# Performance work log

Hardware: AMD Instinct MI355X
Metric: run time of the kernel (lower is better)

The kernel has to match this reference:

```python
import jax, jax.numpy as jnp
import numpy as np

G = 8          # n_games
D_IN = 512     # per-game input dim (equal for all games)
H1 = 1024
H2 = 1024
A = 128        # max_actions
B = 8192       # batch rows


def setup_inputs() -> dict:
    key = jax.random.key(0)
    ks = jax.random.split(key, 9)
    state = jax.random.normal(ks[0], (B, D_IN), dtype=jnp.float32)
    idx = jax.random.randint(ks[1], (B,), 0, G, dtype=jnp.int32)
    # per-game input linears: uniform(-1/sqrt(fan_in), 1/sqrt(fan_in))
    lim1 = 1.0 / np.sqrt(D_IN)
    W1 = jax.random.uniform(ks[2], (G, D_IN, H1), minval=-lim1, maxval=lim1, dtype=jnp.float32)
    b1 = jax.random.uniform(ks[3], (G, H1), minval=-lim1, maxval=lim1, dtype=jnp.float32)
    # shared linear
    lim2 = 1.0 / np.sqrt(H1)
    W2 = jax.random.uniform(ks[4], (H1, H2), minval=-lim2, maxval=lim2, dtype=jnp.float32)
    b2 = jax.random.uniform(ks[5], (H2,), minval=-lim2, maxval=lim2, dtype=jnp.float32)
    # per-game output heads: uniform(-0.003, 0.003)
    W3 = jax.random.uniform(ks[6], (G, H2, A), minval=-0.003, maxval=0.003, dtype=jnp.float32)
    b3 = jax.random.uniform(ks[7], (G, A), minval=-0.003, maxval=0.003, dtype=jnp.float32)
    return {"state": state, "idx": idx, "W1": W1, "b1": b1, "W2": W2, "b2": b2, "W3": W3, "b3": b3}


def reference(state, idx, W1, b1, W2, b2, W3, b3):
    # Torch code concatenates per-game groups in sorted-unique-idx order,
    # i.e. a stable permutation of rows by idx; reproduce exactly.
    perm = jnp.argsort(idx, stable=True)          # [B]
    s = state[perm]                               # [B, D_IN]
    g = idx[perm]                                 # [B] game of each permuted row
    # routed first layer: compute all games then gather per-row game
    h1_all = jnp.einsum('bd,gdh->bgh', s, W1) + b1            # [B, G, H1]
    h1 = jax.nn.relu(jnp.take_along_axis(h1_all, g[:, None, None], axis=1)[:, 0, :])  # [B, H1]
    h_f = jax.nn.relu(h1 @ W2 + b2)                            # [B, H2]
    a = jnp.tanh(jnp.einsum('bh,gha->bga', h_f, W3) + b3)      # [B, G, A]
    # NOTE: original gathers heads with the ORIGINAL (unpermuted) idx,
    # even though rows of `a` are in permuted order. Reproduce faithfully.
    out = jnp.take_along_axis(a, idx[:, None, None], axis=1)[:, 0, :]  # [B, A]
    return out
```

## Files before the change

### kernel.cpp

```cpp
#include <hip/hip_runtime.h>
#include <math.h>

#define G_GAMES 8
#define D_IN 512
#define H1 1024
#define H2 1024
#define A_DIM 128
#define B_ROWS 8192

typedef short bf16x8 __attribute__((ext_vector_type(8)));
typedef float f32x4 __attribute__((ext_vector_type(4)));

#define WS_OFF   0u
#define WS_PERM  256u
#define WS_SPERM 33280u
#define WS_W1T   (WS_SPERM + B_ROWS*D_IN*2u)
#define WS_W2T   (WS_W1T + G_GAMES*D_IN*H1*2u)
#define WS_W3T   (WS_W2T + (unsigned)H1*H2*2u)
#define WS_H1    (WS_W3T + G_GAMES*H2*A_DIM*2u)
#define WS_HF    WS_SPERM

__device__ __forceinline__ unsigned short f2bf(float x) {
  union { float f; unsigned int u; } v; v.f = x;
  unsigned int r = v.u + 0x7fffu + ((v.u >> 16) & 1u);
  return (unsigned short)(r >> 16);
}

__device__ __forceinline__ void async_load16(const void* gptr, void* ldsptr) {
  __builtin_amdgcn_global_load_lds(
      (const __attribute__((address_space(1))) unsigned int*)gptr,
      (__attribute__((address_space(3))) unsigned int*)ldsptr,
      16, 0, 0);
}

__global__ __launch_bounds__(1024) void k_sort(const int* __restrict__ idx,
                                               int* __restrict__ perm,
                                               int* __restrict__ off) {
  __shared__ int wtot[16][9];
  __shared__ int wbase[16][9];
  __shared__ int offs[9];
  const int t = threadIdx.x;
  const int lane = t & 63, wave = t >> 6;
  int my[8];
  {
    const int4 a = *(const int4*)(idx + t * 8);
    const int4 b = *(const int4*)(idx + t * 8 + 4);
    my[0] = a.x; my[1] = a.y; my[2] = a.z; my[3] = a.w;
    my[4] = b.x; my[5] = b.y; my[6] = b.z; my[7] = b.w;
  }
  int local[8] = {0,0,0,0,0,0,0,0};
#pragma unroll
  for (int i = 0; i < 8; ++i) local[my[i]]++;
  int incl[8];
#pragma unroll
  for (int g = 0; g < 8; ++g) {
    int v = local[g];
#pragma unroll
    for (int d = 1; d < 64; d <<= 1) {
      const int n = __shfl_up(v, d);
      if (lane >= d) v += n;
    }
    incl[g] = v;
  }
  if (lane == 63) {
#pragma unroll
    for (int g = 0; g < 8; ++g) wtot[wave][g] = incl[g];
  }
  __syncthreads();
  if (t < 8) {
    int s = 0;
#pragma unroll
    for (int w = 0; w < 16; ++w) { wbase[w][t] = s; s += wtot[w][t]; }
    wtot[0][t] = s;
  }
  __syncthreads();
  if (t == 0) {
    int s = 0;
#pragma unroll
    for (int g = 0; g < 8; ++g) { offs[g] = s; off[g] = s; s += wtot[0][g]; }
    offs[8] = s; off[8] = s;
  }
  __syncthreads();
  int start[8];
#pragma unroll
  for (int g = 0; g < 8; ++g)
    start[g] = offs[g] + wbase[wave][g] + (incl[g] - local[g]);
#pragma unroll
  for (int i = 0; i < 8; ++i) {
    const int g = my[i];
    perm[start[g]++] = t * 8 + i;
  }
}

__device__ __forceinline__ void trans_tile(const float* __restrict__ in,
                                           unsigned short* __restrict__ out,
                                           int R, int C, int xt, int yt, int z) {
  in  += (size_t)z * R * C;
  out += (size_t)z * R * C;
  __shared__ float tile[64][65];
  const int c0 = xt * 64, r0 = yt * 64;
  const int tx = threadIdx.x & 63, ty = threadIdx.x >> 6;
#pragma unroll
  for (int rr = ty; rr < 64; rr += 4)
    tile[rr][tx] = in[(size_t)(r0 + rr) * C + c0 + tx];
  __syncthreads();
#pragma unroll
  for (int cc = ty; cc < 64; cc += 4)
    out[(size_t)(c0 + cc) * R + r0 + tx] = f2bf(tile[tx][cc]);
}

__global__ __launch_bounds__(256) void k_prep(const float* __restrict__ W1,
                                              const float* __restrict__ W2,
                                              const float* __restrict__ W3,
                                              const float* __restrict__ state,
                                              const int* __restrict__ perm,
                                              unsigned short* __restrict__ W1T,
                                              unsigned short* __restrict__ W2T,
                                              unsigned short* __restrict__ W3T,
                                              unsigned short* __restrict__ sPerm) {
  const int b = blockIdx.x;
  if (b < 1024) {
    const int z = b >> 7, r = b & 127;
    trans_tile(W1, W1T, D_IN, H1, r & 15, r >> 4, z);
  } else if (b < 1280) {
    const int r = b - 1024;
    trans_tile(W2, W2T, H1, H2, r & 15, r >> 4, 0);
  } else if (b < 1536) {
    const int r = (b - 1280) & 31, z = (b - 1280) >> 5;
    trans_tile(W3, W3T, H2, A_DIM, r & 1, r >> 1, z);
  } else {
    const int bb = b - 1536;
    const int p = bb * 2 + (threadIdx.x >> 7);
    const int c = (threadIdx.x & 127) << 2;
    const int src = perm[p];
    const float4 v = *(const float4*)(state + (size_t)src * D_IN + c);
    ushort4 o;
    o.x = f2bf(v.x); o.y = f2bf(v.y); o.z = f2bf(v.z); o.w = f2bf(v.w);
    *(ushort4*)(sPerm + (size_t)p * D_IN + c) = o;
  }
}

__device__ __forceinline__ void gemm_mfma_core(const unsigned short* const* aRow,
                                               const unsigned short* const* bRow,
                                               unsigned short* ldsA, unsigned short* ldsB,
                                               int KTOT, int tid, f32x4 acc[4][4]) {
  const int lane = tid & 63;
  const int wave = tid >> 6;
  const int wm = wave & 1, wn = wave >> 1;
  const int gcol = ((lane & 7) ^ (lane >> 3)) << 3;
  char* ldsAc = (char*)ldsA;
  char* ldsBc = (char*)ldsB;
  const int mA = wm * 64 + (lane & 15);
  const int nB = wn * 64 + (lane & 15);
  const int kq = (lane >> 4) & 3;
  const int swz = lane & 7;
  for (int k0 = 0; k0 < KTOT; k0 += 64) {
    __syncthreads();
#pragma unroll
    for (int c = 0; c < 4; ++c) {
      const int ldsRow = wave * 32 + c * 8;
      async_load16(aRow[c] + k0 + gcol, ldsAc + ldsRow * 128);
      async_load16(bRow[c] + k0 + gcol, ldsBc + ldsRow * 128);
    }
    __syncthreads();
#pragma unroll
    for (int ks = 0; ks < 2; ++ks) {
      bf16x8 aF[4], bF[4];
      const int u = ((((ks << 2) + kq) ^ swz) << 4);
#pragma unroll
      for (int i = 0; i < 4; ++i)
        aF[i] = *(const bf16x8*)(ldsAc + (mA + i * 16) * 128 + u);
#pragma unroll
      for (int j = 0; j < 4; ++j)
        bF[j] = *(const bf16x8*)(ldsBc + (nB + j * 16) * 128 + u);
#pragma unroll
      for (int i = 0; i < 4; ++i)
#pragma unroll
        for (int j = 0; j < 4; ++j)
          acc[i][j] = __builtin_amdgcn_mfma_f32_16x16x32_bf16(aF[i], bF[j], acc[i][j], 0, 0, 0);
    }
  }
}

__device__ __forceinline__ bool seg_map(const int* __restrict__ off, int T,
                                        int& g, int& seg1, int& row0) {
  int base = 0;
  for (int gg = 0; gg < 8; ++gg) {
    const int s = off[gg], e = off[gg + 1];
    const int nt = (e - s + 127) >> 7;
    if (T < base + nt) { g = gg; seg1 = e; row0 = s + (T - base) * 128; return true; }
    base += nt;
  }
  return false;
}

__device__ __forceinline__ bool seg_map32(const int* __restrict__ off, int T,
                                          int& g, int& seg1, int& row0) {
  int base = 0;
  for (int gg = 0; gg < 8; ++gg) {
    const int s = off[gg], e = off[gg + 1];
    const int nt = (e - s + 31) >> 5;
    if (T < base + nt) { g = gg; seg1 = e; row0 = s + (T - base) * 32; return true; }
    base += nt;
  }
  return false;
}

__global__ __launch_bounds__(256) void k_gemm1(const unsigned short* __restrict__ sPerm,
                                               const unsigned short* __restrict__ W1T,
                                               const float* __restrict__ b1,
                                               const int* __restrict__ off,
                                               unsigned short* __restrict__ h1out) {
  __shared__ unsigned short ldsA[128 * 64];
  __shared__ unsigned short ldsB[128 * 64];
  int g, seg1, row0;
  if (!seg_map(off, blockIdx.x, g, seg1, row0)) return;
  const int col0 = blockIdx.y * 128;
  const int tid = threadIdx.x, lane = tid & 63, wave = tid >> 6;
  const unsigned short* aRow[4];
  const unsigned short* bRow[4];
#pragma unroll
  for (int c = 0; c < 4; ++c) {
    int r = row0 + wave * 32 + c * 8 + (lane >> 3);
    if (r > seg1 - 1) r = seg1 - 1;
    aRow[c] = sPerm + (size_t)r * D_IN;
    const int nr = col0 + wave * 32 + c * 8 + (lane >> 3);
    bRow[c] = W1T + (size_t)g * H1 * D_IN + (size_t)nr * D_IN;
  }
  f32x4 acc[4][4] = {};
  gemm_mfma_core(aRow, bRow, ldsA, ldsB, D_IN, tid, acc);
  const int wm = wave & 1, wn = wave >> 1;
  const float* bg = b1 + g * H1;
#pragma unroll
  for (int j = 0; j < 4; ++j) {
    const int n = col0 + wn * 64 + j * 16 + (lane & 15);
    const float bj = bg[n];
#pragma unroll
    for (int i = 0; i < 4; ++i) {
      const int rbase = row0 + wm * 64 + i * 16 + ((lane >> 4) << 2);
#pragma unroll
      for (int r = 0; r < 4; ++r) {
        const int p = rbase + r;
        if (p < seg1) {
          float v = acc[i][j][r] + bj;
          v = fmaxf(v, 0.0f);
          h1out[(size_t)p * H1 + n] = f2bf(v);
        }
      }
    }
  }
}

__global__ __launch_bounds__(256) void k_gemm2(const unsigned short* __restrict__ h1in,
                                               const unsigned short* __restrict__ W2T,
                                               const float* __restrict__ b2,
                                               unsigned short* __restrict__ hfout) {
  __shared__ unsigned short ldsA[128 * 64];
  __shared__ unsigned short ldsB[128 * 64];
  const int row0 = blockIdx.x * 128, col0 = blockIdx.y * 128;
  const int tid = threadIdx.x, lane = tid & 63, wave = tid >> 6;
  const unsigned short* aRow[4];
  const unsigned short* bRow[4];
#pragma unroll
  for (int c = 0; c < 4; ++c) {
    const int r = row0 + wave * 32 + c * 8 + (lane >> 3);
    aRow[c] = h1in + (size_t)r * H1;
    const int nr = col0 + wave * 32 + c * 8 + (lane >> 3);
    bRow[c] = W2T + (size_t)nr * H1;
  }
  f32x4 acc[4][4] = {};
  gemm_mfma_core(aRow, bRow, ldsA, ldsB, H1, tid, acc);
  const int wm = wave & 1, wn = wave >> 1;
#pragma unroll
  for (int j = 0; j < 4; ++j) {
    const int n = col0 + wn * 64 + j * 16 + (lane & 15);
    const float bj = b2[n];
#pragma unroll
    for (int i = 0; i < 4; ++i) {
      const int rbase = row0 + wm * 64 + i * 16 + ((lane >> 4) << 2);
#pragma unroll
      for (int r = 0; r < 4; ++r) {
        float v = acc[i][j][r] + bj;
        v = fmaxf(v, 0.0f);
        hfout[(size_t)(rbase + r) * H2 + n] = f2bf(v);
      }
    }
  }
}

__global__ __launch_bounds__(256) void k_gemm3(const unsigned short* __restrict__ hf,
                                               const unsigned short* __restrict__ W3T,
                                               const float* __restrict__ b3,
                                               const int* __restrict__ off,
                                               const int* __restrict__ perm,
                                               float* __restrict__ outp) {
  __shared__ unsigned short ldsA[32 * 64];
  __shared__ unsigned short ldsB[128 * 64];
  int g, seg1, row0;
  if (!seg_map32(off, blockIdx.x, g, seg1, row0)) return;
  const int tid = threadIdx.x, lane = tid & 63, wave = tid >> 6;
  const int wm = wave & 1, wn = wave >> 1;
  const int gcol = ((lane & 7) ^ (lane >> 3)) << 3;
  int q = row0 + wave * 8 + (lane >> 3);
  if (q > seg1 - 1) q = seg1 - 1;
  const unsigned short* aPtr = hf + (size_t)perm[q] * H2;
  const unsigned short* bRow[4];
#pragma unroll
  for (int c = 0; c < 4; ++c) {
    const int nr = wave * 32 + c * 8 + (lane >> 3);
    bRow[c] = W3T + (size_t)g * A_DIM * H2 + (size_t)nr * H2;
  }
  char* ldsAc = (char*)ldsA;
  char* ldsBc = (char*)ldsB;
  const int mA = wm * 16 + (lane & 15);
  const int nB = wn * 64 + (lane & 15);
  const int kq = (lane >> 4) & 3;
  const int swz = lane & 7;
  f32x4 acc[4] = {};
  for (int k0 = 0; k0 < H2; k0 += 64) {
    __syncthreads();
    async_load16(aPtr + k0 + gcol, ldsAc + (wave * 8) * 128);
#pragma unroll
    for (int c = 0; c < 4; ++c)
      async_load16(bRow[c] + k0 + gcol, ldsBc + (wave * 32 + c * 8) * 128);
    __syncthreads();
#pragma unroll
    for (int ks = 0; ks < 2; ++ks) {
      const int u = ((((ks << 2) + kq) ^ swz) << 4);
      const bf16x8 aF = *(const bf16x8*)(ldsAc + mA * 128 + u);
      bf16x8 bF[4];
#pragma unroll
      for (int j = 0; j < 4; ++j)
        bF[j] = *(const bf16x8*)(ldsBc + (nB + j * 16) * 128 + u);
#pragma unroll
      for (int j = 0; j < 4; ++j)
        acc[j] = __builtin_amdgcn_mfma_f32_16x16x32_bf16(aF, bF[j], acc[j], 0, 0, 0);
    }
  }
  const float* bg = b3 + g * A_DIM;
#pragma unroll
  for (int j = 0; j < 4; ++j) {
    const int n = wn * 64 + j * 16 + (lane & 15);
    const float bj = bg[n];
    const int qbase = row0 + wm * 16 + ((lane >> 4) << 2);
#pragma unroll
    for (int r = 0; r < 4; ++r) {
      const int q2 = qbase + r;
      if (q2 < seg1)
        outp[(size_t)perm[q2] * A_DIM + n] = tanhf(acc[j][r] + bj);
    }
  }
}

extern "C" void kernel_launch(void* const* d_in, const int* in_sizes, int n_in,
                              void* d_out, int out_size, void* d_ws, size_t ws_size,
                              hipStream_t stream) {
  (void)in_sizes; (void)n_in; (void)out_size; (void)ws_size;
  const float* state = (const float*)d_in[0];
  const int*   idx   = (const int*)d_in[1];
  const float* W1    = (const float*)d_in[2];
  const float* b1    = (const float*)d_in[3];
  const float* W2    = (const float*)d_in[4];
  const float* b2    = (const float*)d_in[5];
  const float* W3    = (const float*)d_in[6];
  const float* b3    = (const float*)d_in[7];
  float* outp = (float*)d_out;
  char* ws = (char*)d_ws;
  int* off  = (int*)(ws + WS_OFF);
  int* perm = (int*)(ws + WS_PERM);
  unsigned short* sPerm = (unsigned short*)(ws + WS_SPERM);
  unsigned short* W1T   = (unsigned short*)(ws + WS_W1T);
  unsigned short* W2T   = (unsigned short*)(ws + WS_W2T);
  unsigned short* W3T   = (unsigned short*)(ws + WS_W3T);
  unsigned short* h1    = (unsigned short*)(ws + WS_H1);
  unsigned short* hf    = (unsigned short*)(ws + WS_HF);

  hipLaunchKernelGGL(k_sort, dim3(1), dim3(1024), 0, stream, idx, perm, off);
  hipLaunchKernelGGL(k_prep, dim3(1536 + B_ROWS / 2), dim3(256), 0, stream,
                     W1, W2, W3, state, perm, W1T, W2T, W3T, sPerm);
  hipLaunchKernelGGL(k_gemm1, dim3(72, 8), dim3(256), 0, stream, sPerm, W1T, b1, off, h1);
  hipLaunchKernelGGL(k_gemm2, dim3(64, 8), dim3(256), 0, stream, h1, W2T, b2, hf);
  hipLaunchKernelGGL(k_gemm3, dim3(264), dim3(256), 0, stream, hf, W3T, b3, off, perm, outp);
}
```

Baseline: 177.3 us.

## Widen GEMM K-tile to 128 and fold the sort into the weight-prep kernel

```diff
diff --git a/kernel.cpp b/kernel.cpp
--- a/kernel.cpp
+++ b/kernel.cpp
@@ -33,24 +33,21 @@
       16, 0, 0);
 }
 
-__global__ __launch_bounds__(1024) void k_sort(const int* __restrict__ idx,
-                                               int* __restrict__ perm,
-                                               int* __restrict__ off) {
-  __shared__ int wtot[16][9];
-  __shared__ int wbase[16][9];
+__device__ void sort_256(const int* __restrict__ idx, int* __restrict__ perm,
+                         int* __restrict__ off) {
+  __shared__ int wtot[4][9];
+  __shared__ int wbase[4][9];
   __shared__ int offs[9];
-  const int t = threadIdx.x;
-  const int lane = t & 63, wave = t >> 6;
-  int my[8];
-  {
-    const int4 a = *(const int4*)(idx + t * 8);
-    const int4 b = *(const int4*)(idx + t * 8 + 4);
-    my[0] = a.x; my[1] = a.y; my[2] = a.z; my[3] = a.w;
-    my[4] = b.x; my[5] = b.y; my[6] = b.z; my[7] = b.w;
+  const int t = threadIdx.x, lane = t & 63, wave = t >> 6;
+  int my[32];
+#pragma unroll
+  for (int i = 0; i < 8; ++i) {
+    const int4 a = *(const int4*)(idx + t * 32 + i * 4);
+    my[i*4+0] = a.x; my[i*4+1] = a.y; my[i*4+2] = a.z; my[i*4+3] = a.w;
   }
   int local[8] = {0,0,0,0,0,0,0,0};
 #pragma unroll
-  for (int i = 0; i < 8; ++i) local[my[i]]++;
+  for (int i = 0; i < 32; ++i) local[my[i]]++;
   int incl[8];
 #pragma unroll
   for (int g = 0; g < 8; ++g) {
@@ -70,7 +67,7 @@
   if (t < 8) {
     int s = 0;
 #pragma unroll
-    for (int w = 0; w < 16; ++w) { wbase[w][t] = s; s += wtot[w][t]; }
+    for (int w = 0; w < 4; ++w) { wbase[w][t] = s; s += wtot[w][t]; }
     wtot[0][t] = s;
   }
   __syncthreads();
@@ -86,15 +83,15 @@
   for (int g = 0; g < 8; ++g)
     start[g] = offs[g] + wbase[wave][g] + (incl[g] - local[g]);
 #pragma unroll
-  for (int i = 0; i < 8; ++i) {
+  for (int i = 0; i < 32; ++i) {
     const int g = my[i];
-    perm[start[g]++] = t * 8 + i;
-  }
-}
-
-__device__ __forceinline__ void trans_tile(const float* __restrict__ in,
-                                           unsigned short* __restrict__ out,
-                                           int R, int C, int xt, int yt, int z) {
+    perm[start[g]++] = t * 32 + i;
+  }
+}
+
+__device__ void trans_tile(const float* __restrict__ in,
+                           unsigned short* __restrict__ out,
+                           int R, int C, int xt, int yt, int z) {
   in  += (size_t)z * R * C;
   out += (size_t)z * R * C;
   __shared__ float tile[64][65];
@@ -109,15 +106,15 @@
     out[(size_t)(c0 + cc) * R + r0 + tx] = f2bf(tile[tx][cc]);
 }
 
-__global__ __launch_bounds__(256) void k_prep(const float* __restrict__ W1,
+__global__ __launch_bounds__(256) void k_pre1(const float* __restrict__ W1,
                                               const float* __restrict__ W2,
                                               const float* __restrict__ W3,
-                                              const float* __restrict__ state,
-                                              const int* __restrict__ perm,
+                                              const int* __restrict__ idx,
                                               unsigned short* __restrict__ W1T,
                                               unsigned short* __restrict__ W2T,
                                               unsigned short* __restrict__ W3T,
-                                              unsigned short* __restrict__ sPerm) {
+                                              int* __restrict__ perm,
+                                              int* __restrict__ off) {
   const int b = blockIdx.x;
   if (b < 1024) {
     const int z = b >> 7, r = b & 127;
@@ -129,50 +126,50 @@
     const int r = (b - 1280) & 31, z = (b - 1280) >> 5;
     trans_tile(W3, W3T, H2, A_DIM, r & 1, r >> 1, z);
   } else {
-    const int bb = b - 1536;
-    const int p = bb * 2 + (threadIdx.x >> 7);
-    const int c = (threadIdx.x & 127) << 2;
-    const int src = perm[p];
-    const float4 v = *(const float4*)(state + (size_t)src * D_IN + c);
-    ushort4 o;
-    o.x = f2bf(v.x); o.y = f2bf(v.y); o.z = f2bf(v.z); o.w = f2bf(v.w);
-    *(ushort4*)(sPerm + (size_t)p * D_IN + c) = o;
-  }
-}
-
-__device__ __forceinline__ void gemm_mfma_core(const unsigned short* const* aRow,
-                                               const unsigned short* const* bRow,
-                                               unsigned short* ldsA, unsigned short* ldsB,
-                                               int KTOT, int tid, f32x4 acc[4][4]) {
-  const int lane = tid & 63;
-  const int wave = tid >> 6;
+    sort_256(idx, perm, off);
+  }
+}
+
+__global__ __launch_bounds__(256) void k_gather(const float* __restrict__ state,
+                                                const int* __restrict__ perm,
+                                                unsigned short* __restrict__ sPerm) {
+  const int p = blockIdx.x * 2 + (threadIdx.x >> 7);
+  const int c = (threadIdx.x & 127) << 2;
+  const int src = perm[p];
+  const float4 v = *(const float4*)(state + (size_t)src * D_IN + c);
+  ushort4 o;
+  o.x = f2bf(v.x); o.y = f2bf(v.y); o.z = f2bf(v.z); o.w = f2bf(v.w);
+  *(ushort4*)(sPerm + (size_t)p * D_IN + c) = o;
+}
+
+__device__ __forceinline__ void gemm_core128(const unsigned short* const* aP,
+                                             const unsigned short* const* bP,
+                                             char* A, char* Bc,
+                                             int KTOT, int tid, f32x4 acc[4][4]) {
+  const int lane = tid & 63, wave = tid >> 6;
   const int wm = wave & 1, wn = wave >> 1;
-  const int gcol = ((lane & 7) ^ (lane >> 3)) << 3;
-  char* ldsAc = (char*)ldsA;
-  char* ldsBc = (char*)ldsB;
   const int mA = wm * 64 + (lane & 15);
   const int nB = wn * 64 + (lane & 15);
-  const int kq = (lane >> 4) & 3;
-  const int swz = lane & 7;
-  for (int k0 = 0; k0 < KTOT; k0 += 64) {
+  const int quad = lane >> 4;
+  const int sw = lane & 15;
+  for (int k0 = 0; k0 < KTOT; k0 += 128) {
     __syncthreads();
 #pragma unroll
-    for (int c = 0; c < 4; ++c) {
-      const int ldsRow = wave * 32 + c * 8;
-      async_load16(aRow[c] + k0 + gcol, ldsAc + ldsRow * 128);
-      async_load16(bRow[c] + k0 + gcol, ldsBc + ldsRow * 128);
+    for (int c = 0; c < 8; ++c) {
+      const int rbase = wave * 32 + c * 4;
+      async_load16(aP[c] + k0, A + rbase * 256);
+      async_load16(bP[c] + k0, Bc + rbase * 256);
     }
     __syncthreads();
 #pragma unroll
-    for (int ks = 0; ks < 2; ++ks) {
+    for (int ks = 0; ks < 4; ++ks) {
+      const int u = (((ks * 4 + quad) ^ sw) << 4);
       bf16x8 aF[4], bF[4];
-      const int u = ((((ks << 2) + kq) ^ swz) << 4);
-#pragma unroll
-      for (int i = 0; i < 4; ++i)
-        aF[i] = *(const bf16x8*)(ldsAc + (mA + i * 16) * 128 + u);
-#pragma unroll
-      for (int j = 0; j < 4; ++j)
-        bF[j] = *(const bf16x8*)(ldsBc + (nB + j * 16) * 128 + u);
+#pragma unroll
+      for (int i = 0; i < 4; ++i) {
+        aF[i] = *(const bf16x8*)(A + (mA + i * 16) * 256 + u);
+        bF[i] = *(const bf16x8*)(Bc + (nB + i * 16) * 256 + u);
+      }
 #pragma unroll
       for (int i = 0; i < 4; ++i)
 #pragma unroll
@@ -211,33 +208,35 @@
                                                const float* __restrict__ b1,
                                                const int* __restrict__ off,
                                                unsigned short* __restrict__ h1out) {
-  __shared__ unsigned short ldsA[128 * 64];
-  __shared__ unsigned short ldsB[128 * 64];
+  __shared__ unsigned short ldsA[128 * 128];
+  __shared__ unsigned short ldsB[128 * 128];
   int g, seg1, row0;
   if (!seg_map(off, blockIdx.x, g, seg1, row0)) return;
   const int col0 = blockIdx.y * 128;
   const int tid = threadIdx.x, lane = tid & 63, wave = tid >> 6;
-  const unsigned short* aRow[4];
-  const unsigned short* bRow[4];
-#pragma unroll
-  for (int c = 0; c < 4; ++c) {
-    int r = row0 + wave * 32 + c * 8 + (lane >> 3);
-    if (r > seg1 - 1) r = seg1 - 1;
-    aRow[c] = sPerm + (size_t)r * D_IN;
-    const int nr = col0 + wave * 32 + c * 8 + (lane >> 3);
-    bRow[c] = W1T + (size_t)g * H1 * D_IN + (size_t)nr * D_IN;
+  const int quad = lane >> 4, sw = lane & 15;
+  const unsigned short* aP[8];
+  const unsigned short* bP[8];
+#pragma unroll
+  for (int c = 0; c < 8; ++c) {
+    const int rl = wave * 32 + c * 4 + quad;
+    const int srcoff = ((sw ^ (rl & 15)) << 3);
+    int p = row0 + rl;
+    if (p > seg1 - 1) p = seg1 - 1;
+    aP[c] = sPerm + (size_t)p * D_IN + srcoff;
+    bP[c] = W1T + (size_t)g * H1 * D_IN + (size_t)(col0 + rl) * D_IN + srcoff;
   }
   f32x4 acc[4][4] = {};
-  gemm_mfma_core(aRow, bRow, ldsA, ldsB, D_IN, tid, acc);
+  gemm_core128(aP, bP, (char*)ldsA, (char*)ldsB, D_IN, tid, acc);
   const int wm = wave & 1, wn = wave >> 1;
   const float* bg = b1 + g * H1;
 #pragma unroll
   for (int j = 0; j < 4; ++j) {
-    const int n = col0 + wn * 64 + j * 16 + (lane & 15);
+    const int n = col0 + wn * 64 + j * 16 + sw;
     const float bj = bg[n];
 #pragma unroll
     for (int i = 0; i < 4; ++i) {
-      const int rbase = row0 + wm * 64 + i * 16 + ((lane >> 4) << 2);
+      const int rbase = row0 + wm * 64 + i * 16 + (quad << 2);
 #pragma unroll
       for (int r = 0; r < 4; ++r) {
         const int p = rbase + r;
@@ -255,29 +254,30 @@
                                                const unsigned short* __restrict__ W2T,
                                                const float* __restrict__ b2,
                                                unsigned short* __restrict__ hfout) {
-  __shared__ unsigned short ldsA[128 * 64];
-  __shared__ unsigned short ldsB[128 * 64];
+  __shared__ unsigned short ldsA[128 * 128];
+  __shared__ unsigned short ldsB[128 * 128];
   const int row0 = blockIdx.x * 128, col0 = blockIdx.y * 128;
   const int tid = threadIdx.x, lane = tid & 63, wave = tid >> 6;
-  const unsigned short* aRow[4];
-  const unsigned short* bRow[4];
-#pragma unroll
-  for (int c = 0; c < 4; ++c) {
-    const int r = row0 + wave * 32 + c * 8 + (lane >> 3);
-    aRow[c] = h1in + (size_t)r * H1;
-    const int nr = col0 + wave * 32 + c * 8 + (lane >> 3);
-    bRow[c] = W2T + (size_t)nr * H1;
+  const int quad = lane >> 4, sw = lane & 15;
+  const unsigned short* aP[8];
+  const unsigned short* bP[8];
+#pragma unroll
+  for (int c = 0; c < 8; ++c) {
+    const int rl = wave * 32 + c * 4 + quad;
+    const int srcoff = ((sw ^ (rl & 15)) << 3);
+    aP[c] = h1in + (size_t)(row0 + rl) * H1 + srcoff;
+    bP[c] = W2T + (size_t)(col0 + rl) * H1 + srcoff;
   }
   f32x4 acc[4][4] = {};
-  gemm_mfma_core(aRow, bRow, ldsA, ldsB, H1, tid, acc);
+  gemm_core128(aP, bP, (char*)ldsA, (char*)ldsB, H1, tid, acc);
   const int wm = wave & 1, wn = wave >> 1;
 #pragma unroll
   for (int j = 0; j < 4; ++j) {
-    const int n = col0 + wn * 64 + j * 16 + (lane & 15);
+    const int n = col0 + wn * 64 + j * 16 + sw;
     const float bj = b2[n];
 #pragma unroll
     for (int i = 0; i < 4; ++i) {
-      const int rbase = row0 + wm * 64 + i * 16 + ((lane >> 4) << 2);
+      const int rbase = row0 + wm * 64 + i * 16 + (quad << 2);
 #pragma unroll
       for (int r = 0; r < 4; ++r) {
         float v = acc[i][j][r] + bj;
@@ -294,44 +294,51 @@
                                                const int* __restrict__ off,
                                                const int* __restrict__ perm,
                                                float* __restrict__ outp) {
-  __shared__ unsigned short ldsA[32 * 64];
-  __shared__ unsigned short ldsB[128 * 64];
+  __shared__ unsigned short ldsA[32 * 128];
+  __shared__ unsigned short ldsB[128 * 128];
   int g, seg1, row0;
   if (!seg_map32(off, blockIdx.x, g, seg1, row0)) return;
   const int tid = threadIdx.x, lane = tid & 63, wave = tid >> 6;
   const int wm = wave & 1, wn = wave >> 1;
-  const int gcol = ((lane & 7) ^ (lane >> 3)) << 3;
-  int q = row0 + wave * 8 + (lane >> 3);
-  if (q > seg1 - 1) q = seg1 - 1;
-  const unsigned short* aPtr = hf + (size_t)perm[q] * H2;
-  const unsigned short* bRow[4];
-#pragma unroll
-  for (int c = 0; c < 4; ++c) {
-    const int nr = wave * 32 + c * 8 + (lane >> 3);
-    bRow[c] = W3T + (size_t)g * A_DIM * H2 + (size_t)nr * H2;
-  }
-  char* ldsAc = (char*)ldsA;
-  char* ldsBc = (char*)ldsB;
-  const int mA = wm * 16 + (lane & 15);
-  const int nB = wn * 64 + (lane & 15);
-  const int kq = (lane >> 4) & 3;
-  const int swz = lane & 7;
+  const int quad = lane >> 4, sw = lane & 15;
+  const unsigned short* aP[2];
+  const unsigned short* bP[8];
+#pragma unroll
+  for (int c = 0; c < 2; ++c) {
+    const int rl = wave * 8 + c * 4 + quad;
+    const int srcoff = ((sw ^ (rl & 15)) << 3);
+    int q = row0 + rl;
+    if (q > seg1 - 1) q = seg1 - 1;
+    aP[c] = hf + (size_t)perm[q] * H2 + srcoff;
+  }
+#pragma unroll
+  for (int c = 0; c < 8; ++c) {
+    const int rl = wave * 32 + c * 4 + quad;
+    const int srcoff = ((sw ^ (rl & 15)) << 3);
+    bP[c] = W3T + (size_t)g * A_DIM * H2 + (size_t)rl * H2 + srcoff;
+  }
+  char* A = (char*)ldsA;
+  char* Bc = (char*)ldsB;
+  const int mA = wm * 16 + sw;
+  const int nB = wn * 64 + sw;
   f32x4 acc[4] = {};
-  for (int k0 = 0; k0 < H2; k0 += 64) {
+  for (int k0 = 0; k0 < H2; k0 += 128) {
     __syncthreads();
-    async_load16(aPtr + k0 + gcol, ldsAc + (wave * 8) * 128);
-#pragma unroll
-    for (int c = 0; c < 4; ++c)
-      async_load16(bRow[c] + k0 + gcol, ldsBc + (wave * 32 + c * 8) * 128);
+#pragma unroll
+    for (int c = 0; c < 2; ++c)
+      async_load16(aP[c] + k0, A + (wave * 8 + c * 4) * 256);
+#pragma unroll
+    for (int c = 0; c < 8; ++c)
+      async_load16(bP[c] + k0, Bc + (wave * 32 + c * 4) * 256);
     __syncthreads();
 #pragma unroll
-    for (int ks = 0; ks < 2; ++ks) {
-      const int u = ((((ks << 2) + kq) ^ swz) << 4);
-      const bf16x8 aF = *(const bf16x8*)(ldsAc + mA * 128 + u);
+    for (int ks = 0; ks < 4; ++ks) {
+      const int u = (((ks * 4 + quad) ^ sw) << 4);
+      const bf16x8 aF = *(const bf16x8*)(A + mA * 256 + u);
       bf16x8 bF[4];
 #pragma unroll
       for (int j = 0; j < 4; ++j)
-        bF[j] = *(const bf16x8*)(ldsBc + (nB + j * 16) * 128 + u);
+        bF[j] = *(const bf16x8*)(Bc + (nB + j * 16) * 256 + u);
 #pragma unroll
       for (int j = 0; j < 4; ++j)
         acc[j] = __builtin_amdgcn_mfma_f32_16x16x32_bf16(aF, bF[j], acc[j], 0, 0, 0);
@@ -340,9 +347,9 @@
   const float* bg = b3 + g * A_DIM;
 #pragma unroll
   for (int j = 0; j < 4; ++j) {
-    const int n = wn * 64 + j * 16 + (lane & 15);
+    const int n = wn * 64 + j * 16 + sw;
     const float bj = bg[n];
-    const int qbase = row0 + wm * 16 + ((lane >> 4) << 2);
+    const int qbase = row0 + wm * 16 + (quad << 2);
 #pragma unroll
     for (int r = 0; r < 4; ++r) {
       const int q2 = qbase + r;
@@ -375,9 +382,9 @@
   unsigned short* h1    = (unsigned short*)(ws + WS_H1);
   unsigned short* hf    = (unsigned short*)(ws + WS_HF);
 
-  hipLaunchKernelGGL(k_sort, dim3(1), dim3(1024), 0, stream, idx, perm, off);
-  hipLaunchKernelGGL(k_prep, dim3(1536 + B_ROWS / 2), dim3(256), 0, stream,
-                     W1, W2, W3, state, perm, W1T, W2T, W3T, sPerm);
+  hipLaunchKernelGGL(k_pre1, dim3(1537), dim3(256), 0, stream,
+                     W1, W2, W3, idx, W1T, W2T, W3T, perm, off);
+  hipLaunchKernelGGL(k_gather, dim3(B_ROWS / 2), dim3(256), 0, stream, state, perm, sPerm);
   hipLaunchKernelGGL(k_gemm1, dim3(72, 8), dim3(256), 0, stream, sPerm, W1T, b1, off, h1);
   hipLaunchKernelGGL(k_gemm2, dim3(64, 8), dim3(256), 0, stream, h1, W2T, b2, hf);
   hipLaunchKernelGGL(k_gemm3, dim3(264), dim3(256), 0, stream, hf, W3T, b3, off, perm, outp);
```

Result: faster. 172.3 us (-2.8%).
